# Kernel tuning notes

Measured on AMD Instinct MI355X. Metric: run time of the kernel, lower is better.

Reference implementation:

```python
import jax, jax.numpy as jnp
import numpy as np
from jax import lax

B, N, SEG, T = 64, 19, 15, 400
FIN, HID, K, NH, DM, FF, L, NC = 64, 128, 4, 4, 64, 128, 4, 3
EPS = 1e-5


def setup_inputs() -> dict:
    key = jax.random.key(0)
    ks = jax.random.split(key, 40)
    nrm = lambda i, s, sc=0.05: jax.random.normal(ks[i], s, dtype=jnp.float32) * sc
    inp = {
        "X": jax.random.normal(ks[0], (B, N, SEG, T), dtype=jnp.float32),
        "A_hat": jax.random.uniform(ks[1], (B, K, SEG, N, N), dtype=jnp.float32),
        "conv1_w": nrm(2, (32, 1, 25)), "conv1_b": nrm(3, (32,)),
        "conv2_w": nrm(4, (64, 32, 9)), "conv2_b": nrm(5, (64,)),
        "g1_W": nrm(6, (HID, FIN)), "g1_q": nrm(7, (K,), 1.0),
        "g1_bn_g": jnp.ones((HID,)), "g1_bn_b": jnp.zeros((HID,)),
        "g1_bn_m": jnp.zeros((HID,)), "g1_bn_v": jnp.ones((HID,)),
        "g2_W": nrm(8, (FIN, HID)), "g2_q": nrm(9, (K,), 1.0),
        "g2_bn_g": jnp.ones((FIN,)), "g2_bn_b": jnp.zeros((FIN,)),
        "g2_bn_m": jnp.zeros((FIN,)), "g2_bn_v": jnp.ones((FIN,)),
        "cls_token": nrm(10, (1, 1, DM), 0.02), "pos_emb": nrm(11, (1, SEG + 1, DM), 0.02),
        "t_wqkv": nrm(12, (L, 3 * DM, DM)), "t_bqkv": nrm(13, (L, 3 * DM)),
        "t_wo": nrm(14, (L, DM, DM)), "t_bo": nrm(15, (L, DM)),
        "t_ln1g": jnp.ones((L, DM)), "t_ln1b": jnp.zeros((L, DM)),
        "t_w1": nrm(16, (L, FF, DM)), "t_b1": nrm(17, (L, FF)),
        "t_w2": nrm(18, (L, DM, FF)), "t_b2": nrm(19, (L, DM)),
        "t_ln2g": jnp.ones((L, DM)), "t_ln2b": jnp.zeros((L, DM)),
        "clf_w": nrm(20, (NC, DM)), "clf_b": nrm(21, (NC,)),
    }
    return inp


def _ln(x, g, b):
    mu = x.mean(-1, keepdims=True)
    v = ((x - mu) ** 2).mean(-1, keepdims=True)
    return (x - mu) * lax.rsqrt(v + EPS) * g + b


def _maxpool(x, w):  # x: [M, C, T]
    return lax.reduce_window(x, -jnp.inf, lax.max, (1, 1, w), (1, 1, w), "VALID")


def _temporal_encoder(X, c1w, c1b, c2w, c2b):
    # X: [B, SEG, N, T] -> [B, SEG, N, FIN]
    x = X.reshape(-1, 1, T)
    dn = ("NCH", "OIH", "NCH")
    x = lax.conv_general_dilated(x, c1w, (4,), [(12, 12)], dimension_numbers=dn) + c1b[None, :, None]
    x = _maxpool(jax.nn.relu(x), 4)                      # [M,32,25]
    x = lax.conv_general_dilated(x, c2w, (2,), [(4, 4)], dimension_numbers=dn) + c2b[None, :, None]
    x = _maxpool(jax.nn.relu(x), 2)                      # [M,64,6]
    x = x.mean(-1)                                       # AdaptiveAvgPool1d(1)
    return x.reshape(B, SEG, N, FIN)


def _gcn(Xf, A, W, q, g, b, m, v):
    alpha = jax.nn.softmax(q)                            # [K]
    AX = jnp.einsum("bksnm,bsmf->bksnf", A, Xf)          # K-hop diffusion
    Hk = jnp.einsum("bksnf,of->bksno", AX, W)            # shared linear
    H = jnp.einsum("k,bksno->bsno", alpha, Hk)           # attn-weighted hop mix
    H = (H - m) * lax.rsqrt(v + EPS) * g + b             # eval-mode BatchNorm1d
    return jax.nn.relu(H)


def _forward(X, A_hat, conv1_w, conv1_b, conv2_w, conv2_b,
             g1_W, g1_q, g1_bn_g, g1_bn_b, g1_bn_m, g1_bn_v,
             g2_W, g2_q, g2_bn_g, g2_bn_b, g2_bn_m, g2_bn_v,
             cls_token, pos_emb, t_wqkv, t_bqkv, t_wo, t_bo,
             t_ln1g, t_ln1b, t_w1, t_b1, t_w2, t_b2, t_ln2g, t_ln2b,
             clf_w, clf_b):
    Xs = X.reshape(-1, N, SEG, T).transpose(0, 2, 1, 3)  # [B,SEG,N,T]
    feat = _temporal_encoder(Xs, conv1_w, conv1_b, conv2_w, conv2_b)
    H = _gcn(feat, A_hat, g1_W, g1_q, g1_bn_g, g1_bn_b, g1_bn_m, g1_bn_v)
    H = _gcn(H, A_hat, g2_W, g2_q, g2_bn_g, g2_bn_b, g2_bn_m, g2_bn_v)
    g = H.mean(axis=2)                                   # node-mean -> [B,SEG,DM]
    x = jnp.concatenate([jnp.broadcast_to(cls_token, (B, 1, DM)), g], axis=1)
    x = x + pos_emb[:, : SEG + 1]
    dh = DM // NH
    for l in range(L):
        qkv = x @ t_wqkv[l].T + t_bqkv[l]
        qh, kh, vh = [u.reshape(B, SEG + 1, NH, dh).transpose(0, 2, 1, 3)
                      for u in jnp.split(qkv, 3, axis=-1)]
        attn = jax.nn.softmax(jnp.einsum("bhqd,bhkd->bhqk", qh, kh) / jnp.sqrt(jnp.float32(dh)), axis=-1)
        o = jnp.einsum("bhqk,bhkd->bhqd", attn, vh).transpose(0, 2, 1, 3).reshape(B, SEG + 1, DM)
        x = _ln(x + o @ t_wo[l].T + t_bo[l], t_ln1g[l], t_ln1b[l])
        ff = jax.nn.relu(x @ t_w1[l].T + t_b1[l]) @ t_w2[l].T + t_b2[l]
        x = _ln(x + ff, t_ln2g[l], t_ln2b[l])
    return x[:, 0] @ clf_w.T + clf_b                     # [B, NC]


def reference(X, A_hat, conv1_w, conv1_b, conv2_w, conv2_b,
              g1_W, g1_q, g1_bn_g, g1_bn_b, g1_bn_m, g1_bn_v,
              g2_W, g2_q, g2_bn_g, g2_bn_b, g2_bn_m, g2_bn_v,
              cls_token, pos_emb, t_wqkv, t_bqkv, t_wo, t_bo,
              t_ln1g, t_ln1b, t_w1, t_b1, t_w2, t_b2, t_ln2g, t_ln2b,
              clf_w, clf_b):
    return _forward(X, A_hat, conv1_w, conv1_b, conv2_w, conv2_b,
                    g1_W, g1_q, g1_bn_g, g1_bn_b, g1_bn_m, g1_bn_v,
                    g2_W, g2_q, g2_bn_g, g2_bn_b, g2_bn_m, g2_bn_v,
                    cls_token, pos_emb, t_wqkv, t_bqkv, t_wo, t_bo,
                    t_ln1g, t_ln1b, t_w1, t_b1, t_w2, t_b2, t_ln2g, t_ln2b,
                    clf_w, clf_b)
```

## Files before the change

### kernel.cpp

```cpp
#include <hip/hip_runtime.h>
#include <cmath>

#define B_ 64
#define N_ 19
#define SEG_ 15
#define T_ 400
#define FIN_ 64
#define HID_ 128
#define K_ 4
#define NH_ 4
#define DM_ 64
#define FF_ 128
#define L_ 4
#define NC_ 3
#define EPS_ 1e-5f

typedef __attribute__((ext_vector_type(8))) short bf16x8;
typedef __attribute__((ext_vector_type(4))) short bf16x4;
typedef __attribute__((ext_vector_type(4))) float f32x4;
typedef unsigned short ushort_t;

__device__ __forceinline__ ushort_t f2bf(float x) {
  union { float f; unsigned u; } a; a.f = x;
  unsigned r = a.u + 0x7fffu + ((a.u >> 16) & 1u);
  return (ushort_t)(r >> 16);
}
__device__ __forceinline__ float bf2f(ushort_t h) {
  union { unsigned u; float f; } a; a.u = ((unsigned)h) << 16;
  return a.f;
}

__global__ __launch_bounds__(256) void k_prep(
    const float* __restrict__ c1w, const float* __restrict__ c2w,
    const float* __restrict__ wqkv, const float* __restrict__ wo,
    const float* __restrict__ w1, const float* __restrict__ w2,
    const float* __restrict__ g1W, const float* __restrict__ g2W,
    ushort_t* __restrict__ bt,
    ushort_t* __restrict__ Th, ushort_t* __restrict__ Tl,
    ushort_t* __restrict__ W1h, ushort_t* __restrict__ W1l,
    ushort_t* __restrict__ W2h, ushort_t* __restrict__ W2l,
    ushort_t* __restrict__ C1h, ushort_t* __restrict__ C1l) {
  int gid = blockIdx.x * 256 + threadIdx.x;
  if (gid < 18944) {
    int oc = gid / 296, k = gid - oc * 296;
    int ic = k & 31, kk = k >> 5;
    ushort_t v = 0;
    if (kk < 9) v = f2bf(c2w[oc * 288 + ic * 9 + kk]);
    bt[gid] = v;
  } else if (gid < 68096) {
    int i = gid - 18944;
    int l = i / 12288, r = i % 12288;
    float v = wqkv[i];
    ushort_t h = f2bf(v);
    int dst = l * 32768 + r;
    Th[dst] = h; Tl[dst] = f2bf(v - bf2f(h));
  } else if (gid < 84480) {
    int i = gid - 68096;
    int l = i / 4096, r = i % 4096;
    float v = wo[i];
    ushort_t h = f2bf(v);
    int dst = l * 32768 + 12288 + r;
    Th[dst] = h; Tl[dst] = f2bf(v - bf2f(h));
  } else if (gid < 117248) {
    int i = gid - 84480;
    int l = i / 8192, r = i % 8192;
    float v = w1[i];
    ushort_t h = f2bf(v);
    int dst = l * 32768 + 16384 + r;
    Th[dst] = h; Tl[dst] = f2bf(v - bf2f(h));
  } else if (gid < 150016) {
    int i = gid - 117248;
    int l = i / 8192, r = i % 8192;
    float v = w2[i];
    ushort_t h = f2bf(v);
    int dst = l * 32768 + 24576 + r;
    Th[dst] = h; Tl[dst] = f2bf(v - bf2f(h));
  } else if (gid < 158208) {
    int i = gid - 150016;
    float v = g1W[i];
    ushort_t h = f2bf(v);
    W1h[i] = h;
    W1l[i] = f2bf(v - bf2f(h));
  } else if (gid < 166400) {
    int i = gid - 158208;
    float v = g2W[i];
    ushort_t h = f2bf(v);
    W2h[i] = h;
    W2l[i] = f2bf(v - bf2f(h));
  } else if (gid < 167424) {
    int i = gid - 166400;
    int oc = i >> 5, kk = i & 31;
    float v = (kk < 25) ? c1w[oc * 25 + kk] : 0.f;
    ushort_t h = f2bf(v);
    C1h[i] = h;
    C1l[i] = f2bf(v - bf2f(h));
  }
}

#define RPB 4
#define ICP 40
#define P1R 40
#define OFF_XPH 0
#define OFF_XPL 3840
#define OFF_P1  7680
#define SMEM_T  20480

__global__ __launch_bounds__(256, 4) void k_temporal(
    const float* __restrict__ X, const float* __restrict__ c1b,
    const float* __restrict__ c2b,
    const ushort_t* __restrict__ C1h, const ushort_t* __restrict__ C1l,
    const ushort_t* __restrict__ BmatT, float* __restrict__ Xf) {
  __shared__ __align__(16) unsigned char smem[SMEM_T];
  ushort_t* xph = (ushort_t*)(smem + OFF_XPH);
  ushort_t* xpl = (ushort_t*)(smem + OFF_XPL);
  ushort_t* p1T = (ushort_t*)(smem + OFF_P1);
  float* Dbuf = (float*)smem;

  const int tid = threadIdx.x;
  const int row0 = blockIdx.x * RPB;
  const int lane = tid & 63, wv = tid >> 6;
  const int quad = lane >> 4, nl = lane & 15;

  for (int i = tid; i < 3200; i += 256) ((unsigned*)p1T)[i] = 0u;
  for (int r = 0; r < RPB; ++r) {
    const int gr = row0 + r;
    const int n = gr % N_;
    const int s = (gr / N_) % SEG_;
    const int b = gr / (N_ * SEG_);
    const float* xin = X + (((size_t)b * N_ + n) * SEG_ + s) * T_ - 12;
    for (int i = tid; i < 480; i += 256) {
      float v = (i >= 12 && i < 412) ? xin[i] : 0.f;
      ushort_t h = f2bf(v);
      xph[r * 480 + i] = h;
      xpl[r * 480 + i] = f2bf(v - bf2f(h));
    }
  }
  __syncthreads();

  {
    bf16x8 bh0 = *(const bf16x8*)(C1h + nl * 32 + quad * 8);
    bf16x8 bh1 = *(const bf16x8*)(C1h + (16 + nl) * 32 + quad * 8);
    bf16x8 bl0 = *(const bf16x8*)(C1l + nl * 32 + quad * 8);
    bf16x8 bl1 = *(const bf16x8*)(C1l + (16 + nl) * 32 + quad * 8);
    const float bias0 = c1b[nl], bias1 = c1b[16 + nl];
    for (int t = wv; t < 28; t += 4) {
      const int r = t / 7, mt = t - r * 7;
      const int aoff = r * 480 + mt * 64 + nl * 4 + quad * 8;
      union { bf16x4 q[2]; bf16x8 v; } ah, al;
      ah.q[0] = *(const bf16x4*)(xph + aoff);
      ah.q[1] = *(const bf16x4*)(xph + aoff + 4);
      al.q[0] = *(const bf16x4*)(xpl + aoff);
      al.q[1] = *(const bf16x4*)(xpl + aoff + 4);
      f32x4 a0 = (f32x4){0.f, 0.f, 0.f, 0.f};
      a0 = __builtin_amdgcn_mfma_f32_16x16x32_bf16(ah.v, bh0, a0, 0, 0, 0);
      a0 = __builtin_amdgcn_mfma_f32_16x16x32_bf16(al.v, bh0, a0, 0, 0, 0);
      a0 = __builtin_amdgcn_mfma_f32_16x16x32_bf16(ah.v, bl0, a0, 0, 0, 0);
      f32x4 a1 = (f32x4){0.f, 0.f, 0.f, 0.f};
      a1 = __builtin_amdgcn_mfma_f32_16x16x32_bf16(ah.v, bh1, a1, 0, 0, 0);
      a1 = __builtin_amdgcn_mfma_f32_16x16x32_bf16(al.v, bh1, a1, 0, 0, 0);
      a1 = __builtin_amdgcn_mfma_f32_16x16x32_bf16(ah.v, bl1, a1, 0, 0, 0);
      const int j = mt * 4 + quad;
      if (j < 25) {
        float m0 = fmaxf(fmaxf(a0[0], a0[1]), fmaxf(a0[2], a0[3]));
        float m1 = fmaxf(fmaxf(a1[0], a1[1]), fmaxf(a1[2], a1[3]));
        p1T[(r * P1R + j + 4) * ICP + nl] = f2bf(fmaxf(m0 + bias0, 0.f));
        p1T[(r * P1R + j + 4) * ICP + 16 + nl] = f2bf(fmaxf(m1 + bias1, 0.f));
      }
    }
  }
  __syncthreads();

  f32x4 acc[4];
  int abase[4];
#pragma unroll
  for (int tm = 0; tm < 4; ++tm) {
    acc[tm] = (f32x4){0.f, 0.f, 0.f, 0.f};
    int m = tm * 16 + nl;
    int rl = m / 14;
    int op = m - rl * 14;
    if (rl > 3) rl = 3;
    if (op > 13) op = 13;
    abase[tm] = (rl * P1R + 2 * op) * ICP + quad * 8;
  }
  const ushort_t* brow = BmatT + (wv * 16 + nl) * 296 + quad * 8;
#pragma unroll
  for (int kk = 0; kk < 9; ++kk) {
    bf16x8 bfr = *(const bf16x8*)(brow + kk * 32);
#pragma unroll
    for (int tm = 0; tm < 4; ++tm) {
      bf16x8 afr = *(const bf16x8*)(p1T + abase[tm] + kk * ICP);
      acc[tm] = __builtin_amdgcn_mfma_f32_16x16x32_bf16(afr, bfr, acc[tm], 0, 0, 0);
    }
  }
  __syncthreads();

#pragma unroll
  for (int tm = 0; tm < 4; ++tm)
#pragma unroll
    for (int rg = 0; rg < 4; ++rg)
      Dbuf[(tm * 16 + quad * 4 + rg) * 66 + wv * 16 + nl] = acc[tm][rg];
  __syncthreads();

  for (int o = tid; o < RPB * 64; o += 256) {
    int rl = o >> 6, oc = o & 63;
    float bias = c2b[oc];
    const float* dr = Dbuf + (rl * 14) * 66 + oc;
    float s = 0.f;
#pragma unroll
    for (int jj = 0; jj < 6; ++jj) {
      float v = fmaxf(dr[(2 * jj) * 66], dr[(2 * jj + 1) * 66]) + bias;
      s += fmaxf(v, 0.f);
    }
    Xf[(size_t)(row0 + rl) * FIN_ + oc] = s * (1.f / 6.f);
  }
}

__global__ __launch_bounds__(256) void k_gcn(
    const float* __restrict__ A, const float* __restrict__ Xf,
    const ushort_t* __restrict__ W1h, const ushort_t* __restrict__ W1l,
    const ushort_t* __restrict__ W2h, const ushort_t* __restrict__ W2l,
    const float* __restrict__ q1, const float* __restrict__ q2,
    const float* __restrict__ b1g, const float* __restrict__ b1b,
    const float* __restrict__ b1m, const float* __restrict__ b1v,
    const float* __restrict__ b2g, const float* __restrict__ b2b,
    const float* __restrict__ b2m, const float* __restrict__ b2v,
    float* __restrict__ G) {
  const int bs = blockIdx.x;
  const int b = bs / SEG_;
  const int s = bs % SEG_;
  const int tid = threadIdx.x;

  __shared__ __align__(16) ushort_t xh[32 * 72], xl[32 * 72];
  __shared__ __align__(16) ushort_t Hh[32 * 136], Hl[32 * 136];
  __shared__ float abar1[N_ * N_], abar2[N_ * N_];
  __shared__ float ybuf[N_ * 130];
  __shared__ float zbuf[N_ * 64];
  __shared__ float sc1[HID_], sh1[HID_], sc2[FIN_], sh2[FIN_];

  {
    float p0 = q1[0], p1 = q1[1], p2 = q1[2], p3 = q1[3];
    float mx = fmaxf(fmaxf(p0, p1), fmaxf(p2, p3));
    float e0 = expf(p0 - mx), e1 = expf(p1 - mx), e2 = expf(p2 - mx), e3 = expf(p3 - mx);
    float inv = 1.f / (e0 + e1 + e2 + e3);
    float a0 = e0 * inv, a1 = e1 * inv, a2 = e2 * inv, a3 = e3 * inv;
    float r0 = q2[0], r1 = q2[1], r2 = q2[2], r3 = q2[3];
    float mx2 = fmaxf(fmaxf(r0, r1), fmaxf(r2, r3));
    float f0 = expf(r0 - mx2), f1 = expf(r1 - mx2), f2 = expf(r2 - mx2), f3 = expf(r3 - mx2);
    float inv2 = 1.f / (f0 + f1 + f2 + f3);
    float c0 = f0 * inv2, c1 = f1 * inv2, c2 = f2 * inv2, c3 = f3 * inv2;
    const size_t kstride = (size_t)SEG_ * N_ * N_;
    const float* Ab = A + ((size_t)b * K_ * SEG_ + s) * (N_ * N_);
    for (int i = tid; i < N_ * N_; i += 256) {
      float v0 = Ab[i], v1 = Ab[i + kstride], v2 = Ab[i + 2 * kstride], v3 = Ab[i + 3 * kstride];
      abar1[i] = a0 * v0 + a1 * v1 + a2 * v2 + a3 * v3;
      abar2[i] = c0 * v0 + c1 * v1 + c2 * v2 + c3 * v3;
    }
  }

  for (int i = tid; i < 32 * 72 / 2; i += 256) {
    ((unsigned*)xh)[i] = 0u; ((unsigned*)xl)[i] = 0u;
  }
  for (int i = tid; i < 32 * 136 / 2; i += 256) {
    ((unsigned*)Hh)[i] = 0u; ((unsigned*)Hl)[i] = 0u;
  }
  for (int o = tid; o < HID_; o += 256) {
    float sc = b1g[o] * rsqrtf(b1v[o] + EPS_);
    sc1[o] = sc; sh1[o] = b1b[o] - b1m[o] * sc;
  }
  for (int o = tid; o < FIN_; o += 256) {
    float sc = b2g[o] * rsqrtf(b2v[o] + EPS_);
    sc2[o] = sc; sh2[o] = b2b[o] - b2m[o] * sc;
  }
  __syncthreads();

  const float* xb = Xf + (size_t)bs * N_ * FIN_;
  for (int i = tid; i < N_ * FIN_; i += 256) {
    int r = i >> 6, f = i & 63;
    float v = xb[i];
    ushort_t h = f2bf(v);
    xh[r * 72 + f] = h;
    xl[r * 72 + f] = f2bf(v - bf2f(h));
  }
  __syncthreads();

  const int lane = tid & 63, wv = tid >> 6;
  const int quad = lane >> 4, nl = lane & 15;

#pragma unroll
  for (int mt = 0; mt < 2; ++mt) {
#pragma unroll
    for (int ntl = 0; ntl < 2; ++ntl) {
      const int nt = wv * 2 + ntl;
      f32x4 acc = (f32x4){0.f, 0.f, 0.f, 0.f};
#pragma unroll
      for (int ks = 0; ks < 2; ++ks) {
        bf16x8 ah = *(const bf16x8*)(xh + (mt * 16 + nl) * 72 + ks * 32 + quad * 8);
        bf16x8 al = *(const bf16x8*)(xl + (mt * 16 + nl) * 72 + ks * 32 + quad * 8);
        bf16x8 bh = *(const bf16x8*)(W1h + (nt * 16 + nl) * 64 + ks * 32 + quad * 8);
        bf16x8 bl = *(const bf16x8*)(W1l + (nt * 16 + nl) * 64 + ks * 32 + quad * 8);
        acc = __builtin_amdgcn_mfma_f32_16x16x32_bf16(ah, bh, acc, 0, 0, 0);
        acc = __builtin_amdgcn_mfma_f32_16x16x32_bf16(al, bh, acc, 0, 0, 0);
        acc = __builtin_amdgcn_mfma_f32_16x16x32_bf16(ah, bl, acc, 0, 0, 0);
      }
#pragma unroll
      for (int r = 0; r < 4; ++r) {
        int m = mt * 16 + quad * 4 + r;
        if (m < N_) ybuf[m * 130 + nt * 16 + nl] = acc[r];
      }
    }
  }
  __syncthreads();

  for (int idx = tid; idx < N_ * HID_; idx += 256) {
    int nn = idx >> 7, o = idx & 127;
    float acc = 0.f;
    const float* ar = &abar1[nn * N_];
#pragma unroll
    for (int m = 0; m < N_; ++m) acc += ar[m] * ybuf[m * 130 + o];
    float h = fmaxf(acc * sc1[o] + sh1[o], 0.f);
    ushort_t hh = f2bf(h);
    Hh[nn * 136 + o] = hh;
    Hl[nn * 136 + o] = f2bf(h - bf2f(hh));
  }
  __syncthreads();

  {
    const int nt = wv;
#pragma unroll
    for (int mt = 0; mt < 2; ++mt) {
      f32x4 acc = (f32x4){0.f, 0.f, 0.f, 0.f};
#pragma unroll
      for (int ks = 0; ks < 4; ++ks) {
        bf16x8 ah = *(const bf16x8*)(Hh + (mt * 16 + nl) * 136 + ks * 32 + quad * 8);
        bf16x8 al = *(const bf16x8*)(Hl + (mt * 16 + nl) * 136 + ks * 32 + quad * 8);
        bf16x8 bh = *(const bf16x8*)(W2h + (nt * 16 + nl) * 128 + ks * 32 + quad * 8);
        bf16x8 bl = *(const bf16x8*)(W2l + (nt * 16 + nl) * 128 + ks * 32 + quad * 8);
        acc = __builtin_amdgcn_mfma_f32_16x16x32_bf16(ah, bh, acc, 0, 0, 0);
        acc = __builtin_amdgcn_mfma_f32_16x16x32_bf16(al, bh, acc, 0, 0, 0);
        acc = __builtin_amdgcn_mfma_f32_16x16x32_bf16(ah, bl, acc, 0, 0, 0);
      }
#pragma unroll
      for (int r = 0; r < 4; ++r) {
        int m = mt * 16 + quad * 4 + r;
        if (m < N_) ybuf[m * 66 + nt * 16 + nl] = acc[r];
      }
    }
  }
  __syncthreads();

  for (int idx = tid; idx < N_ * FIN_; idx += 256) {
    int nn = idx >> 6, o = idx & 63;
    float acc = 0.f;
    const float* ar = &abar2[nn * N_];
#pragma unroll
    for (int m = 0; m < N_; ++m) acc += ar[m] * ybuf[m * 66 + o];
    zbuf[idx] = fmaxf(acc * sc2[o] + sh2[o], 0.f);
  }
  __syncthreads();

  if (tid < FIN_) {
    float ssum = 0.f;
#pragma unroll
    for (int nn = 0; nn < N_; ++nn) ssum += zbuf[nn * 64 + tid];
    G[(size_t)bs * FIN_ + tid] = ssum * (1.f / (float)N_);
  }
}

__global__ __launch_bounds__(256, 1) void k_transformer(
    const float* __restrict__ G, const float* __restrict__ cls,
    const float* __restrict__ pos,
    const ushort_t* __restrict__ Th, const ushort_t* __restrict__ Tl,
    const float* __restrict__ bqkv, const float* __restrict__ bo,
    const float* __restrict__ ln1g, const float* __restrict__ ln1b,
    const float* __restrict__ b1, const float* __restrict__ b2,
    const float* __restrict__ ln2g, const float* __restrict__ ln2b,
    const float* __restrict__ clfw, const float* __restrict__ clfb,
    float* __restrict__ out) {
  const int b = blockIdx.x;
  const int tid = threadIdx.x;
  const int lane = tid & 63, wv = tid >> 6;
  const int quad = lane >> 4, nl = lane & 15;

  __shared__ float xbuf[16 * 64];
  __shared__ __align__(16) ushort_t xh[16 * 72], xl[16 * 72];
  __shared__ float qkvb[16 * 196];
  __shared__ float scb[NH_ * 272];
  __shared__ __align__(16) ushort_t oh[16 * 72], ol[16 * 72];
  __shared__ __align__(16) ushort_t h1h[16 * 136], h1l[16 * 136];
  __shared__ float tmpb[16 * 64];

  for (int i = tid; i < 16 * 64; i += 256) {
    int t = i >> 6, d = i & 63;
    float base = (t == 0) ? cls[d] : G[((size_t)b * SEG_ + (t - 1)) * DM_ + d];
    float v = base + pos[t * DM_ + d];
    xbuf[i] = v;
    ushort_t h = f2bf(v);
    xh[t * 72 + d] = h;
    xl[t * 72 + d] = f2bf(v - bf2f(h));
  }
  __syncthreads();

  for (int l = 0; l < L_; ++l) {
    const ushort_t* TH = Th + l * 32768;
    const ushort_t* TL = Tl + l * 32768;

    bf16x8 qwh[3][2], qwl[3][2];
#pragma unroll
    for (int ntl = 0; ntl < 3; ++ntl)
#pragma unroll
      for (int ks = 0; ks < 2; ++ks) {
        const int nt = wv * 3 + ntl;
        qwh[ntl][ks] = *(const bf16x8*)(TH + (nt * 16 + nl) * 64 + ks * 32 + quad * 8);
        qwl[ntl][ks] = *(const bf16x8*)(TL + (nt * 16 + nl) * 64 + ks * 32 + quad * 8);
      }
    bf16x8 owh[2], owl[2];
#pragma unroll
    for (int ks = 0; ks < 2; ++ks) {
      owh[ks] = *(const bf16x8*)(TH + 12288 + (wv * 16 + nl) * 64 + ks * 32 + quad * 8);
      owl[ks] = *(const bf16x8*)(TL + 12288 + (wv * 16 + nl) * 64 + ks * 32 + quad * 8);
    }
    bf16x8 f1h[2][2], f1l[2][2];
#pragma unroll
    for (int ntl = 0; ntl < 2; ++ntl)
#pragma unroll
      for (int ks = 0; ks < 2; ++ks) {
        const int nt = wv * 2 + ntl;
        f1h[ntl][ks] = *(const bf16x8*)(TH + 16384 + (nt * 16 + nl) * 64 + ks * 32 + quad * 8);
        f1l[ntl][ks] = *(const bf16x8*)(TL + 16384 + (nt * 16 + nl) * 64 + ks * 32 + quad * 8);
      }
    bf16x8 f2h[4], f2l[4];
#pragma unroll
    for (int ks = 0; ks < 4; ++ks) {
      f2h[ks] = *(const bf16x8*)(TH + 24576 + (wv * 16 + nl) * 128 + ks * 32 + quad * 8);
      f2l[ks] = *(const bf16x8*)(TL + 24576 + (wv * 16 + nl) * 128 + ks * 32 + quad * 8);
    }

#pragma unroll
    for (int ntl = 0; ntl < 3; ++ntl) {
      const int nt = wv * 3 + ntl;
      f32x4 acc = (f32x4){0.f, 0.f, 0.f, 0.f};
#pragma unroll
      for (int ks = 0; ks < 2; ++ks) {
        bf16x8 ah = *(const bf16x8*)(xh + nl * 72 + ks * 32 + quad * 8);
        bf16x8 al = *(const bf16x8*)(xl + nl * 72 + ks * 32 + quad * 8);
        acc = __builtin_amdgcn_mfma_f32_16x16x32_bf16(ah, qwh[ntl][ks], acc, 0, 0, 0);
        acc = __builtin_amdgcn_mfma_f32_16x16x32_bf16(al, qwh[ntl][ks], acc, 0, 0, 0);
        acc = __builtin_amdgcn_mfma_f32_16x16x32_bf16(ah, qwl[ntl][ks], acc, 0, 0, 0);
      }
      const int j = nt * 16 + nl;
      const float bias = bqkv[l * 192 + j];
#pragma unroll
      for (int r = 0; r < 4; ++r)
        qkvb[(quad * 4 + r) * 196 + j] = acc[r] + bias;
    }
    __syncthreads();

    {
      const int h = wv;
      float sc[4];
      const float* qr = &qkvb[nl * 196 + h * 16];
#pragma unroll
      for (int uu = 0; uu < 4; ++uu) {
        const float* kr = &qkvb[(quad * 4 + uu) * 196 + 64 + h * 16];
        float a = 0.f;
#pragma unroll
        for (int d = 0; d < 16; ++d) a += qr[d] * kr[d];
        sc[uu] = a * 0.25f;
      }
      float mx = fmaxf(fmaxf(sc[0], sc[1]), fmaxf(sc[2], sc[3]));
      mx = fmaxf(mx, __shfl_xor(mx, 16));
      mx = fmaxf(mx, __shfl_xor(mx, 32));
      float e[4];
      float sum = 0.f;
#pragma unroll
      for (int uu = 0; uu < 4; ++uu) { e[uu] = expf(sc[uu] - mx); sum += e[uu]; }
      sum += __shfl_xor(sum, 16);
      sum += __shfl_xor(sum, 32);
      const float is = 1.f / sum;
      float* prow = &scb[h * 272 + nl * 17];
#pragma unroll
      for (int uu = 0; uu < 4; ++uu) prow[quad * 4 + uu] = e[uu] * is;
      float o[4] = {0.f, 0.f, 0.f, 0.f};
      for (int u = 0; u < 16; ++u) {
        float p = prow[u];
        const float* vr = &qkvb[u * 196 + 128 + h * 16 + quad * 4];
#pragma unroll
        for (int dd = 0; dd < 4; ++dd) o[dd] += p * vr[dd];
      }
      const int eb = h * 16 + quad * 4;
#pragma unroll
      for (int dd = 0; dd < 4; ++dd) {
        ushort_t hh = f2bf(o[dd]);
        oh[nl * 72 + eb + dd] = hh;
        ol[nl * 72 + eb + dd] = f2bf(o[dd] - bf2f(hh));
      }
    }
    __syncthreads();

    {
      f32x4 acc = (f32x4){0.f, 0.f, 0.f, 0.f};
#pragma unroll
      for (int ks = 0; ks < 2; ++ks) {
        bf16x8 ah = *(const bf16x8*)(oh + nl * 72 + ks * 32 + quad * 8);
        bf16x8 al = *(const bf16x8*)(ol + nl * 72 + ks * 32 + quad * 8);
        acc = __builtin_amdgcn_mfma_f32_16x16x32_bf16(ah, owh[ks], acc, 0, 0, 0);
        acc = __builtin_amdgcn_mfma_f32_16x16x32_bf16(al, owh[ks], acc, 0, 0, 0);
        acc = __builtin_amdgcn_mfma_f32_16x16x32_bf16(ah, owl[ks], acc, 0, 0, 0);
      }
      const int d = wv * 16 + nl;
      const float bias = bo[l * 64 + d];
#pragma unroll
      for (int r = 0; r < 4; ++r) {
        int t = quad * 4 + r;
        tmpb[t * 64 + d] = xbuf[t * 64 + d] + acc[r] + bias;
      }
    }
    __syncthreads();

    {
      int t = tid >> 4, i2 = tid & 15;
      float4 v = ((const float4*)(tmpb + t * 64))[i2];
      float s = v.x + v.y + v.z + v.w;
      s += __shfl_xor(s, 1); s += __shfl_xor(s, 2);
      s += __shfl_xor(s, 4); s += __shfl_xor(s, 8);
      float mu = s * (1.f / 64.f);
      float d0 = v.x - mu, d1 = v.y - mu, d2 = v.z - mu, d3 = v.w - mu;
      float vr = d0 * d0 + d1 * d1 + d2 * d2 + d3 * d3;
      vr += __shfl_xor(vr, 1); vr += __shfl_xor(vr, 2);
      vr += __shfl_xor(vr, 4); vr += __shfl_xor(vr, 8);
      float rs = rsqrtf(vr * (1.f / 64.f) + EPS_);
      float4 g4 = ((const float4*)(ln1g + l * 64))[i2];
      float4 b4 = ((const float4*)(ln1b + l * 64))[i2];
      float4 o4;
      o4.x = d0 * rs * g4.x + b4.x; o4.y = d1 * rs * g4.y + b4.y;
      o4.z = d2 * rs * g4.z + b4.z; o4.w = d3 * rs * g4.w + b4.w;
      ((float4*)(xbuf + t * 64))[i2] = o4;
      int base = t * 72 + i2 * 4;
      ushort_t h0 = f2bf(o4.x), h1 = f2bf(o4.y), h2 = f2bf(o4.z), h3 = f2bf(o4.w);
      xh[base + 0] = h0; xh[base + 1] = h1; xh[base + 2] = h2; xh[base + 3] = h3;
      xl[base + 0] = f2bf(o4.x - bf2f(h0));
      xl[base + 1] = f2bf(o4.y - bf2f(h1));
      xl[base + 2] = f2bf(o4.z - bf2f(h2));
      xl[base + 3] = f2bf(o4.w - bf2f(h3));
    }
    __syncthreads();

#pragma unroll
    for (int ntl = 0; ntl < 2; ++ntl) {
      const int nt = wv * 2 + ntl;
      f32x4 acc = (f32x4){0.f, 0.f, 0.f, 0.f};
#pragma unroll
      for (int ks = 0; ks < 2; ++ks) {
        bf16x8 ah = *(const bf16x8*)(xh + nl * 72 + ks * 32 + quad * 8);
        bf16x8 al = *(const bf16x8*)(xl + nl * 72 + ks * 32 + quad * 8);
        acc = __builtin_amdgcn_mfma_f32_16x16x32_bf16(ah, f1h[ntl][ks], acc, 0, 0, 0);
        acc = __builtin_amdgcn_mfma_f32_16x16x32_bf16(al, f1h[ntl][ks], acc, 0, 0, 0);
        acc = __builtin_amdgcn_mfma_f32_16x16x32_bf16(ah, f1l[ntl][ks], acc, 0, 0, 0);
      }
      const int f = nt * 16 + nl;
      const float bias = b1[l * 128 + f];
#pragma unroll
      for (int r = 0; r < 4; ++r) {
        int t = quad * 4 + r;
        float v = fmaxf(acc[r] + bias, 0.f);
        ushort_t hh = f2bf(v);
        h1h[t * 136 + f] = hh;
        h1l[t * 136 + f] = f2bf(v - bf2f(hh));
      }
    }
    __syncthreads();

    {
      f32x4 acc = (f32x4){0.f, 0.f, 0.f, 0.f};
#pragma unroll
      for (int ks = 0; ks < 4; ++ks) {
        bf16x8 ah = *(const bf16x8*)(h1h + nl * 136 + ks * 32 + quad * 8);
        bf16x8 al = *(const bf16x8*)(h1l + nl * 136 + ks * 32 + quad * 8);
        acc = __builtin_amdgcn_mfma_f32_16x16x32_bf16(ah, f2h[ks], acc, 0, 0, 0);
        acc = __builtin_amdgcn_mfma_f32_16x16x32_bf16(al, f2h[ks], acc, 0, 0, 0);
        acc = __builtin_amdgcn_mfma_f32_16x16x32_bf16(ah, f2l[ks], acc, 0, 0, 0);
      }
      const int d = wv * 16 + nl;
      const float bias = b2[l * 64 + d];
#pragma unroll
      for (int r = 0; r < 4; ++r) {
        int t = quad * 4 + r;
        tmpb[t * 64 + d] = xbuf[t * 64 + d] + acc[r] + bias;
      }
    }
    __syncthreads();

    {
      int t = tid >> 4, i2 = tid & 15;
      float4 v = ((const float4*)(tmpb + t * 64))[i2];
      float s = v.x + v.y + v.z + v.w;
      s += __shfl_xor(s, 1); s += __shfl_xor(s, 2);
      s += __shfl_xor(s, 4); s += __shfl_xor(s, 8);
      float mu = s * (1.f / 64.f);
      float d0 = v.x - mu, d1 = v.y - mu, d2 = v.z - mu, d3 = v.w - mu;
      float vr = d0 * d0 + d1 * d1 + d2 * d2 + d3 * d3;
      vr += __shfl_xor(vr, 1); vr += __shfl_xor(vr, 2);
      vr += __shfl_xor(vr, 4); vr += __shfl_xor(vr, 8);
      float rs = rsqrtf(vr * (1.f / 64.f) + EPS_);
      float4 g4 = ((const float4*)(ln2g + l * 64))[i2];
      float4 b4 = ((const float4*)(ln2b + l * 64))[i2];
      float4 o4;
      o4.x = d0 * rs * g4.x + b4.x; o4.y = d1 * rs * g4.y + b4.y;
      o4.z = d2 * rs * g4.z + b4.z; o4.w = d3 * rs * g4.w + b4.w;
      ((float4*)(xbuf + t * 64))[i2] = o4;
      int base = t * 72 + i2 * 4;
      ushort_t h0 = f2bf(o4.x), h1 = f2bf(o4.y), h2 = f2bf(o4.z), h3 = f2bf(o4.w);
      xh[base + 0] = h0; xh[base + 1] = h1; xh[base + 2] = h2; xh[base + 3] = h3;
      xl[base + 0] = f2bf(o4.x - bf2f(h0));
      xl[base + 1] = f2bf(o4.y - bf2f(h1));
      xl[base + 2] = f2bf(o4.z - bf2f(h2));
      xl[base + 3] = f2bf(o4.w - bf2f(h3));
    }
    __syncthreads();
  }

  if (tid < NC_) {
    float acc = clfb[tid];
    const float* wr = &clfw[tid * DM_];
    for (int d = 0; d < DM_; ++d) acc += xbuf[d] * wr[d];
    out[b * NC_ + tid] = acc;
  }
}

extern "C" void kernel_launch(void* const* d_in, const int* in_sizes, int n_in,
                              void* d_out, int out_size, void* d_ws, size_t ws_size,
                              hipStream_t stream) {
  (void)in_sizes; (void)n_in; (void)out_size; (void)ws_size;
  const float* X    = (const float*)d_in[0];
  const float* A    = (const float*)d_in[1];
  const float* c1w  = (const float*)d_in[2];
  const float* c1b  = (const float*)d_in[3];
  const float* c2w  = (const float*)d_in[4];
  const float* c2b  = (const float*)d_in[5];
  const float* g1W  = (const float*)d_in[6];
  const float* g1q  = (const float*)d_in[7];
  const float* g1g  = (const float*)d_in[8];
  const float* g1b  = (const float*)d_in[9];
  const float* g1m  = (const float*)d_in[10];
  const float* g1v  = (const float*)d_in[11];
  const float* g2W  = (const float*)d_in[12];
  const float* g2q  = (const float*)d_in[13];
  const float* g2g  = (const float*)d_in[14];
  const float* g2b  = (const float*)d_in[15];
  const float* g2m  = (const float*)d_in[16];
  const float* g2v  = (const float*)d_in[17];
  const float* cls  = (const float*)d_in[18];
  const float* pos  = (const float*)d_in[19];
  const float* wqkv = (const float*)d_in[20];
  const float* bqkv = (const float*)d_in[21];
  const float* wo   = (const float*)d_in[22];
  const float* bo   = (const float*)d_in[23];
  const float* ln1g = (const float*)d_in[24];
  const float* ln1b = (const float*)d_in[25];
  const float* w1   = (const float*)d_in[26];
  const float* b1   = (const float*)d_in[27];
  const float* w2   = (const float*)d_in[28];
  const float* b2   = (const float*)d_in[29];
  const float* ln2g = (const float*)d_in[30];
  const float* ln2b = (const float*)d_in[31];
  const float* clfw = (const float*)d_in[32];
  const float* clfb = (const float*)d_in[33];
  float* out = (float*)d_out;

  char* wsb = (char*)d_ws;
  ushort_t* BmatT = (ushort_t*)(wsb + 0);
  ushort_t* Th  = (ushort_t*)(wsb + 37888);
  ushort_t* Tl  = (ushort_t*)(wsb + 300032);
  ushort_t* W1h = (ushort_t*)(wsb + 562176);
  ushort_t* W1l = (ushort_t*)(wsb + 578560);
  ushort_t* W2h = (ushort_t*)(wsb + 594944);
  ushort_t* W2l = (ushort_t*)(wsb + 611328);
  ushort_t* C1h = (ushort_t*)(wsb + 627712);
  ushort_t* C1l = (ushort_t*)(wsb + 629760);
  float* Xf   = (float*)(wsb + 631808);
  float* G    = (float*)(wsb + 5301248);

  k_prep<<<654, 256, 0, stream>>>(c1w, c2w, wqkv, wo, w1, w2, g1W, g2W,
                                  BmatT, Th, Tl, W1h, W1l, W2h, W2l, C1h, C1l);
  k_temporal<<<B_ * SEG_ * N_ / RPB, 256, 0, stream>>>(
      X, c1b, c2b, C1h, C1l, BmatT, Xf);
  k_gcn<<<B_ * SEG_, 256, 0, stream>>>(A, Xf, W1h, W1l, W2h, W2l,
                                       g1q, g2q, g1g, g1b, g1m, g1v,
                                       g2g, g2b, g2m, g2v, G);
  k_transformer<<<B_, 256, 0, stream>>>(G, cls, pos, Th, Tl,
                                        bqkv, bo, ln1g, ln1b, b1, b2, ln2g, ln2b,
                                        clfw, clfb, out);
}
```

Measured before the change: 216.3 us.

## Fuse temporal conv encoder into GCN kernel and stage transformer params in LDS

The temporal conv kernel is merged into the GCN kernel. Each (b,s) block now computes conv features for its 19 nodes in 5 chunks of up to 4 rows and writes them straight into the bf16 hi/lo shared buffers, so the Xf round trip through global memory and one launch are gone. The transformer kernel also preloads all per-layer biases, LayerNorm params and classifier weights into shared memory. In exchange, parallelism drops: 960 blocks each loop serially over 5 chunks instead of 3420 small blocks, and the larger shared memory footprint lowers occupancy (launch bounds 256,2).

```diff
diff --git a/kernel.cpp b/kernel.cpp
--- a/kernel.cpp
+++ b/kernel.cpp
@@ -97,126 +97,14 @@
   }
 }
 
-#define RPB 4
 #define ICP 40
 #define P1R 40
-#define OFF_XPH 0
-#define OFF_XPL 3840
-#define OFF_P1  7680
-#define SMEM_T  20480
-
-__global__ __launch_bounds__(256, 4) void k_temporal(
-    const float* __restrict__ X, const float* __restrict__ c1b,
-    const float* __restrict__ c2b,
+
+__global__ __launch_bounds__(256, 2) void k_tg(
+    const float* __restrict__ X, const float* __restrict__ A,
+    const float* __restrict__ c1b, const float* __restrict__ c2b,
     const ushort_t* __restrict__ C1h, const ushort_t* __restrict__ C1l,
-    const ushort_t* __restrict__ BmatT, float* __restrict__ Xf) {
-  __shared__ __align__(16) unsigned char smem[SMEM_T];
-  ushort_t* xph = (ushort_t*)(smem + OFF_XPH);
-  ushort_t* xpl = (ushort_t*)(smem + OFF_XPL);
-  ushort_t* p1T = (ushort_t*)(smem + OFF_P1);
-  float* Dbuf = (float*)smem;
-
-  const int tid = threadIdx.x;
-  const int row0 = blockIdx.x * RPB;
-  const int lane = tid & 63, wv = tid >> 6;
-  const int quad = lane >> 4, nl = lane & 15;
-
-  for (int i = tid; i < 3200; i += 256) ((unsigned*)p1T)[i] = 0u;
-  for (int r = 0; r < RPB; ++r) {
-    const int gr = row0 + r;
-    const int n = gr % N_;
-    const int s = (gr / N_) % SEG_;
-    const int b = gr / (N_ * SEG_);
-    const float* xin = X + (((size_t)b * N_ + n) * SEG_ + s) * T_ - 12;
-    for (int i = tid; i < 480; i += 256) {
-      float v = (i >= 12 && i < 412) ? xin[i] : 0.f;
-      ushort_t h = f2bf(v);
-      xph[r * 480 + i] = h;
-      xpl[r * 480 + i] = f2bf(v - bf2f(h));
-    }
-  }
-  __syncthreads();
-
-  {
-    bf16x8 bh0 = *(const bf16x8*)(C1h + nl * 32 + quad * 8);
-    bf16x8 bh1 = *(const bf16x8*)(C1h + (16 + nl) * 32 + quad * 8);
-    bf16x8 bl0 = *(const bf16x8*)(C1l + nl * 32 + quad * 8);
-    bf16x8 bl1 = *(const bf16x8*)(C1l + (16 + nl) * 32 + quad * 8);
-    const float bias0 = c1b[nl], bias1 = c1b[16 + nl];
-    for (int t = wv; t < 28; t += 4) {
-      const int r = t / 7, mt = t - r * 7;
-      const int aoff = r * 480 + mt * 64 + nl * 4 + quad * 8;
-      union { bf16x4 q[2]; bf16x8 v; } ah, al;
-      ah.q[0] = *(const bf16x4*)(xph + aoff);
-      ah.q[1] = *(const bf16x4*)(xph + aoff + 4);
-      al.q[0] = *(const bf16x4*)(xpl + aoff);
-      al.q[1] = *(const bf16x4*)(xpl + aoff + 4);
-      f32x4 a0 = (f32x4){0.f, 0.f, 0.f, 0.f};
-      a0 = __builtin_amdgcn_mfma_f32_16x16x32_bf16(ah.v, bh0, a0, 0, 0, 0);
-      a0 = __builtin_amdgcn_mfma_f32_16x16x32_bf16(al.v, bh0, a0, 0, 0, 0);
-      a0 = __builtin_amdgcn_mfma_f32_16x16x32_bf16(ah.v, bl0, a0, 0, 0, 0);
-      f32x4 a1 = (f32x4){0.f, 0.f, 0.f, 0.f};
-      a1 = __builtin_amdgcn_mfma_f32_16x16x32_bf16(ah.v, bh1, a1, 0, 0, 0);
-      a1 = __builtin_amdgcn_mfma_f32_16x16x32_bf16(al.v, bh1, a1, 0, 0, 0);
-      a1 = __builtin_amdgcn_mfma_f32_16x16x32_bf16(ah.v, bl1, a1, 0, 0, 0);
-      const int j = mt * 4 + quad;
-      if (j < 25) {
-        float m0 = fmaxf(fmaxf(a0[0], a0[1]), fmaxf(a0[2], a0[3]));
-        float m1 = fmaxf(fmaxf(a1[0], a1[1]), fmaxf(a1[2], a1[3]));
-        p1T[(r * P1R + j + 4) * ICP + nl] = f2bf(fmaxf(m0 + bias0, 0.f));
-        p1T[(r * P1R + j + 4) * ICP + 16 + nl] = f2bf(fmaxf(m1 + bias1, 0.f));
-      }
-    }
-  }
-  __syncthreads();
-
-  f32x4 acc[4];
-  int abase[4];
-#pragma unroll
-  for (int tm = 0; tm < 4; ++tm) {
-    acc[tm] = (f32x4){0.f, 0.f, 0.f, 0.f};
-    int m = tm * 16 + nl;
-    int rl = m / 14;
-    int op = m - rl * 14;
-    if (rl > 3) rl = 3;
-    if (op > 13) op = 13;
-    abase[tm] = (rl * P1R + 2 * op) * ICP + quad * 8;
-  }
-  const ushort_t* brow = BmatT + (wv * 16 + nl) * 296 + quad * 8;
-#pragma unroll
-  for (int kk = 0; kk < 9; ++kk) {
-    bf16x8 bfr = *(const bf16x8*)(brow + kk * 32);
-#pragma unroll
-    for (int tm = 0; tm < 4; ++tm) {
-      bf16x8 afr = *(const bf16x8*)(p1T + abase[tm] + kk * ICP);
-      acc[tm] = __builtin_amdgcn_mfma_f32_16x16x32_bf16(afr, bfr, acc[tm], 0, 0, 0);
-    }
-  }
-  __syncthreads();
-
-#pragma unroll
-  for (int tm = 0; tm < 4; ++tm)
-#pragma unroll
-    for (int rg = 0; rg < 4; ++rg)
-      Dbuf[(tm * 16 + quad * 4 + rg) * 66 + wv * 16 + nl] = acc[tm][rg];
-  __syncthreads();
-
-  for (int o = tid; o < RPB * 64; o += 256) {
-    int rl = o >> 6, oc = o & 63;
-    float bias = c2b[oc];
-    const float* dr = Dbuf + (rl * 14) * 66 + oc;
-    float s = 0.f;
-#pragma unroll
-    for (int jj = 0; jj < 6; ++jj) {
-      float v = fmaxf(dr[(2 * jj) * 66], dr[(2 * jj + 1) * 66]) + bias;
-      s += fmaxf(v, 0.f);
-    }
-    Xf[(size_t)(row0 + rl) * FIN_ + oc] = s * (1.f / 6.f);
-  }
-}
-
-__global__ __launch_bounds__(256) void k_gcn(
-    const float* __restrict__ A, const float* __restrict__ Xf,
+    const ushort_t* __restrict__ BmatT,
     const ushort_t* __restrict__ W1h, const ushort_t* __restrict__ W1l,
     const ushort_t* __restrict__ W2h, const ushort_t* __restrict__ W2l,
     const float* __restrict__ q1, const float* __restrict__ q2,
@@ -229,6 +117,14 @@
   const int b = bs / SEG_;
   const int s = bs % SEG_;
   const int tid = threadIdx.x;
+  const int lane = tid & 63, wv = tid >> 6;
+  const int quad = lane >> 4, nl = lane & 15;
+
+  __shared__ __align__(16) unsigned char tsm[20480];
+  ushort_t* xph = (ushort_t*)tsm;
+  ushort_t* xpl = (ushort_t*)(tsm + 3840);
+  ushort_t* p1T = (ushort_t*)(tsm + 7680);
+  float* Dbuf = (float*)tsm;
 
   __shared__ __align__(16) ushort_t xh[32 * 72], xl[32 * 72];
   __shared__ __align__(16) ushort_t Hh[32 * 136], Hl[32 * 136];
@@ -273,18 +169,105 @@
   }
   __syncthreads();
 
-  const float* xb = Xf + (size_t)bs * N_ * FIN_;
-  for (int i = tid; i < N_ * FIN_; i += 256) {
-    int r = i >> 6, f = i & 63;
-    float v = xb[i];
-    ushort_t h = f2bf(v);
-    xh[r * 72 + f] = h;
-    xl[r * 72 + f] = f2bf(v - bf2f(h));
-  }
-  __syncthreads();
-
-  const int lane = tid & 63, wv = tid >> 6;
-  const int quad = lane >> 4, nl = lane & 15;
+  for (int ch = 0; ch < 5; ++ch) {
+    const int r0 = ch * 4;
+    const int nrows = (r0 + 4 <= N_) ? 4 : (N_ - r0);
+
+    for (int i = tid; i < 3200; i += 256) ((unsigned*)p1T)[i] = 0u;
+    for (int r = 0; r < nrows; ++r) {
+      const int n = r0 + r;
+      const float* xin = X + (((size_t)b * N_ + n) * SEG_ + s) * T_ - 12;
+      for (int i = tid; i < 480; i += 256) {
+        float v = (i >= 12 && i < 412) ? xin[i] : 0.f;
+        ushort_t h = f2bf(v);
+        xph[r * 480 + i] = h;
+        xpl[r * 480 + i] = f2bf(v - bf2f(h));
+      }
+    }
+    __syncthreads();
+
+    {
+      bf16x8 bh0 = *(const bf16x8*)(C1h + nl * 32 + quad * 8);
+      bf16x8 bh1 = *(const bf16x8*)(C1h + (16 + nl) * 32 + quad * 8);
+      bf16x8 bl0 = *(const bf16x8*)(C1l + nl * 32 + quad * 8);
+      bf16x8 bl1 = *(const bf16x8*)(C1l + (16 + nl) * 32 + quad * 8);
+      const float bias0 = c1b[nl], bias1 = c1b[16 + nl];
+      for (int t = wv; t < 28; t += 4) {
+        const int r = t / 7, mt = t - r * 7;
+        if (r >= nrows) continue;
+        const int aoff = r * 480 + mt * 64 + nl * 4 + quad * 8;
+        union { bf16x4 q[2]; bf16x8 v; } ah, al;
+        ah.q[0] = *(const bf16x4*)(xph + aoff);
+        ah.q[1] = *(const bf16x4*)(xph + aoff + 4);
+        al.q[0] = *(const bf16x4*)(xpl + aoff);
+        al.q[1] = *(const bf16x4*)(xpl + aoff + 4);
+        f32x4 a0 = (f32x4){0.f, 0.f, 0.f, 0.f};
+        a0 = __builtin_amdgcn_mfma_f32_16x16x32_bf16(ah.v, bh0, a0, 0, 0, 0);
+        a0 = __builtin_amdgcn_mfma_f32_16x16x32_bf16(al.v, bh0, a0, 0, 0, 0);
+        a0 = __builtin_amdgcn_mfma_f32_16x16x32_bf16(ah.v, bl0, a0, 0, 0, 0);
+        f32x4 a1 = (f32x4){0.f, 0.f, 0.f, 0.f};
+        a1 = __builtin_amdgcn_mfma_f32_16x16x32_bf16(ah.v, bh1, a1, 0, 0, 0);
+        a1 = __builtin_amdgcn_mfma_f32_16x16x32_bf16(al.v, bh1, a1, 0, 0, 0);
+        a1 = __builtin_amdgcn_mfma_f32_16x16x32_bf16(ah.v, bl1, a1, 0, 0, 0);
+        const int j = mt * 4 + quad;
+        if (j < 25) {
+          float m0 = fmaxf(fmaxf(a0[0], a0[1]), fmaxf(a0[2], a0[3]));
+          float m1 = fmaxf(fmaxf(a1[0], a1[1]), fmaxf(a1[2], a1[3]));
+          p1T[(r * P1R + j + 4) * ICP + nl] = f2bf(fmaxf(m0 + bias0, 0.f));
+          p1T[(r * P1R + j + 4) * ICP + 16 + nl] = f2bf(fmaxf(m1 + bias1, 0.f));
+        }
+      }
+    }
+    __syncthreads();
+
+    f32x4 acc[4];
+    int abase[4];
+#pragma unroll
+    for (int tm = 0; tm < 4; ++tm) {
+      acc[tm] = (f32x4){0.f, 0.f, 0.f, 0.f};
+      int m = tm * 16 + nl;
+      int rl = m / 14;
+      int op = m - rl * 14;
+      if (rl > 3) rl = 3;
+      if (op > 13) op = 13;
+      abase[tm] = (rl * P1R + 2 * op) * ICP + quad * 8;
+    }
+    const ushort_t* brow = BmatT + (wv * 16 + nl) * 296 + quad * 8;
+#pragma unroll
+    for (int kk = 0; kk < 9; ++kk) {
+      bf16x8 bfr = *(const bf16x8*)(brow + kk * 32);
+#pragma unroll
+      for (int tm = 0; tm < 4; ++tm) {
+        bf16x8 afr = *(const bf16x8*)(p1T + abase[tm] + kk * ICP);
+        acc[tm] = __builtin_amdgcn_mfma_f32_16x16x32_bf16(afr, bfr, acc[tm], 0, 0, 0);
+      }
+    }
+    __syncthreads();
+
+#pragma unroll
+    for (int tm = 0; tm < 4; ++tm)
+#pragma unroll
+      for (int rg = 0; rg < 4; ++rg)
+        Dbuf[(tm * 16 + quad * 4 + rg) * 66 + wv * 16 + nl] = acc[tm][rg];
+    __syncthreads();
+
+    for (int o = tid; o < nrows * 64; o += 256) {
+      int rl = o >> 6, oc = o & 63;
+      float bias = c2b[oc];
+      const float* dr = Dbuf + (rl * 14) * 66 + oc;
+      float sum = 0.f;
+#pragma unroll
+      for (int jj = 0; jj < 6; ++jj) {
+        float v = fmaxf(dr[(2 * jj) * 66], dr[(2 * jj + 1) * 66]) + bias;
+        sum += fmaxf(v, 0.f);
+      }
+      float xv = sum * (1.f / 6.f);
+      ushort_t h = f2bf(xv);
+      xh[(r0 + rl) * 72 + oc] = h;
+      xl[(r0 + rl) * 72 + oc] = f2bf(xv - bf2f(h));
+    }
+    __syncthreads();
+  }
 
 #pragma unroll
   for (int mt = 0; mt < 2; ++mt) {
@@ -388,6 +371,24 @@
   __shared__ __align__(16) ushort_t oh[16 * 72], ol[16 * 72];
   __shared__ __align__(16) ushort_t h1h[16 * 136], h1l[16 * 136];
   __shared__ float tmpb[16 * 64];
+  __shared__ __align__(16) float pbuf[L_ * 704];
+  __shared__ __align__(16) float cw[200];
+
+  for (int i = tid; i < L_ * 704; i += 256) {
+    int l = i / 704, r = i - l * 704;
+    float v;
+    if (r < 192)       v = bqkv[l * 192 + r];
+    else if (r < 256)  v = bo[l * 64 + r - 192];
+    else if (r < 384)  v = b1[l * 128 + r - 256];
+    else if (r < 448)  v = b2[l * 64 + r - 384];
+    else if (r < 512)  v = ln1g[l * 64 + r - 448];
+    else if (r < 576)  v = ln1b[l * 64 + r - 512];
+    else if (r < 640)  v = ln2g[l * 64 + r - 576];
+    else               v = ln2b[l * 64 + r - 640];
+    pbuf[i] = v;
+  }
+  if (tid < 192) cw[tid] = clfw[tid];
+  if (tid < NC_) cw[192 + tid] = clfb[tid];
 
   for (int i = tid; i < 16 * 64; i += 256) {
     int t = i >> 6, d = i & 63;
@@ -403,6 +404,7 @@
   for (int l = 0; l < L_; ++l) {
     const ushort_t* TH = Th + l * 32768;
     const ushort_t* TL = Tl + l * 32768;
+    const float* P = pbuf + l * 704;
 
     bf16x8 qwh[3][2], qwl[3][2];
 #pragma unroll
@@ -448,7 +450,7 @@
         acc = __builtin_amdgcn_mfma_f32_16x16x32_bf16(ah, qwl[ntl][ks], acc, 0, 0, 0);
       }
       const int j = nt * 16 + nl;
-      const float bias = bqkv[l * 192 + j];
+      const float bias = P[j];
 #pragma unroll
       for (int r = 0; r < 4; ++r)
         qkvb[(quad * 4 + r) * 196 + j] = acc[r] + bias;
@@ -508,7 +510,7 @@
         acc = __builtin_amdgcn_mfma_f32_16x16x32_bf16(ah, owl[ks], acc, 0, 0, 0);
       }
       const int d = wv * 16 + nl;
-      const float bias = bo[l * 64 + d];
+      const float bias = P[192 + d];
 #pragma unroll
       for (int r = 0; r < 4; ++r) {
         int t = quad * 4 + r;
@@ -529,8 +531,8 @@
       vr += __shfl_xor(vr, 1); vr += __shfl_xor(vr, 2);
       vr += __shfl_xor(vr, 4); vr += __shfl_xor(vr, 8);
       float rs = rsqrtf(vr * (1.f / 64.f) + EPS_);
-      float4 g4 = ((const float4*)(ln1g + l * 64))[i2];
-      float4 b4 = ((const float4*)(ln1b + l * 64))[i2];
+      float4 g4 = ((const float4*)(P + 448))[i2];
+      float4 b4 = ((const float4*)(P + 512))[i2];
       float4 o4;
       o4.x = d0 * rs * g4.x + b4.x; o4.y = d1 * rs * g4.y + b4.y;
       o4.z = d2 * rs * g4.z + b4.z; o4.w = d3 * rs * g4.w + b4.w;
@@ -558,7 +560,7 @@
         acc = __builtin_amdgcn_mfma_f32_16x16x32_bf16(ah, f1l[ntl][ks], acc, 0, 0, 0);
       }
       const int f = nt * 16 + nl;
-      const float bias = b1[l * 128 + f];
+      const float bias = P[256 + f];
 #pragma unroll
       for (int r = 0; r < 4; ++r) {
         int t = quad * 4 + r;
@@ -581,7 +583,7 @@
         acc = __builtin_amdgcn_mfma_f32_16x16x32_bf16(ah, f2l[ks], acc, 0, 0, 0);
       }
       const int d = wv * 16 + nl;
-      const float bias = b2[l * 64 + d];
+      const float bias = P[384 + d];
 #pragma unroll
       for (int r = 0; r < 4; ++r) {
         int t = quad * 4 + r;
@@ -602,8 +604,8 @@
       vr += __shfl_xor(vr, 1); vr += __shfl_xor(vr, 2);
       vr += __shfl_xor(vr, 4); vr += __shfl_xor(vr, 8);
       float rs = rsqrtf(vr * (1.f / 64.f) + EPS_);
-      float4 g4 = ((const float4*)(ln2g + l * 64))[i2];
-      float4 b4 = ((const float4*)(ln2b + l * 64))[i2];
+      float4 g4 = ((const float4*)(P + 576))[i2];
+      float4 b4 = ((const float4*)(P + 640))[i2];
       float4 o4;
       o4.x = d0 * rs * g4.x + b4.x; o4.y = d1 * rs * g4.y + b4.y;
       o4.z = d2 * rs * g4.z + b4.z; o4.w = d3 * rs * g4.w + b4.w;
@@ -620,8 +622,8 @@
   }
 
   if (tid < NC_) {
-    float acc = clfb[tid];
-    const float* wr = &clfw[tid * DM_];
+    float acc = cw[192 + tid];
+    const float* wr = &cw[tid * DM_];
     for (int d = 0; d < DM_; ++d) acc += xbuf[d] * wr[d];
     out[b * NC_ + tid] = acc;
   }
@@ -677,16 +679,14 @@
   ushort_t* W2l = (ushort_t*)(wsb + 611328);
   ushort_t* C1h = (ushort_t*)(wsb + 627712);
   ushort_t* C1l = (ushort_t*)(wsb + 629760);
-  float* Xf   = (float*)(wsb + 631808);
-  float* G    = (float*)(wsb + 5301248);
+  float* G    = (float*)(wsb + 631808);
 
   k_prep<<<654, 256, 0, stream>>>(c1w, c2w, wqkv, wo, w1, w2, g1W, g2W,
                                   BmatT, Th, Tl, W1h, W1l, W2h, W2l, C1h, C1l);
-  k_temporal<<<B_ * SEG_ * N_ / RPB, 256, 0, stream>>>(
-      X, c1b, c2b, C1h, C1l, BmatT, Xf);
-  k_gcn<<<B_ * SEG_, 256, 0, stream>>>(A, Xf, W1h, W1l, W2h, W2l,
-                                       g1q, g2q, g1g, g1b, g1m, g1v,
-                                       g2g, g2b, g2m, g2v, G);
+  k_tg<<<B_ * SEG_, 256, 0, stream>>>(X, A, c1b, c2b, C1h, C1l, BmatT,
+                                      W1h, W1l, W2h, W2l, g1q, g2q,
+                                      g1g, g1b, g1m, g1v,
+                                      g2g, g2b, g2m, g2v, G);
   k_transformer<<<B_, 256, 0, stream>>>(G, cls, pos, Th, Tl,
                                         bqkv, bo, ln1g, ln1b, b1, b2, ln2g, ln2b,
                                         clfw, clfb, out);
```

Result: slower. 246.9 us (+14.2%).
